# Optimization experiments

Hardware: AMD Instinct MI355X
Metric: run time of the kernel (lower is better)

The kernel has to match this reference:

```python
import jax, jax.numpy as jnp
import numpy as np

B, C_IN, H, W = 8, 64, 128, 128
NUM_POINT = 128
N_INST = 512
INIT_STRIDE, COARSE_STRIDE, DOWN_SAMPLE = 10.0, 4.0, 4.0
D_MODEL, N_HEADS = 256, 8


def conv2d(x, w, b, pad):
    y = jax.lax.conv_general_dilated(x, w, (1, 1), [(pad, pad), (pad, pad)],
                                     dimension_numbers=('NCHW', 'OIHW', 'NCHW'))
    return y + b[None, :, None, None]


def trans_feature(x, w1, b1, w2, b2):
    # Conv3x3 -> ReLU -> Conv1x1 (c_in -> 256 -> 254)
    return conv2d(jax.nn.relu(conv2d(x, w1, b1, 1)), w2, b2, 0)


def grid_sample_points(feat, img_idx, pts):
    # get_gcn_feature: per-instance bilinear sampling of feat[img_idx] at pixel
    # coords pts. torch grid_sample(align_corners=False, padding_mode='zeros');
    # the normalize->unnormalize of pixel coords collapses to a -0.5 shift.
    Bf, C, Hf, Wf = feat.shape
    ix = pts[..., 0] - 0.5
    iy = pts[..., 1] - 0.5
    x0 = jnp.floor(ix)
    y0 = jnp.floor(iy)
    wx = ix - x0
    wy = iy - y0

    def gather(yy, xx, wgt):
        valid = (xx >= 0) & (xx < Wf) & (yy >= 0) & (yy < Hf)
        xc = jnp.clip(xx, 0, Wf - 1).astype(jnp.int32)
        yc = jnp.clip(yy, 0, Hf - 1).astype(jnp.int32)
        v = feat[img_idx[:, None], :, yc, xc]  # [N,P,C]
        return v * (wgt * valid)[..., None]

    return (gather(y0, x0, (1 - wx) * (1 - wy)) + gather(y0, x0 + 1, wx * (1 - wy))
            + gather(y0 + 1, x0, (1 - wx) * wy) + gather(y0 + 1, x0 + 1, wx * wy))


def normalize_poly(poly):
    # Center each contour and scale by its max extent -> positional encoding in [-1,1]
    mean = poly.mean(axis=1, keepdims=True)
    p = poly - mean
    scale = jnp.max(jnp.abs(p), axis=(1, 2), keepdims=True) + 1e-6
    return p / scale


def csa(x, wqkv, bqkv, wo, bo, whead, bhead):
    # ContourSelfAttention: MHSA over contour points + linear head to 2D offsets
    N, P, C = x.shape
    d = C // N_HEADS
    qkv = x @ wqkv + bqkv
    q, k, v = jnp.split(qkv, 3, axis=-1)
    sh = lambda t: t.reshape(N, P, N_HEADS, d).transpose(0, 2, 1, 3)
    q, k, v = sh(q), sh(k), sh(v)
    attn = jax.nn.softmax(jnp.einsum('nhpd,nhqd->nhpq', q, k) / jnp.sqrt(jnp.float32(d)), axis=-1)
    o = jnp.einsum('nhpq,nhqd->nhpd', attn, v).transpose(0, 2, 1, 3).reshape(N, P, C)
    o = o @ wo + bo
    return o @ whead + bhead  # [N,P,2]


def setup_inputs():
    key = jax.random.key(0)
    ks = jax.random.split(key, 32)
    s = 0.05
    inp = {
        'cnn_feature': jax.random.normal(ks[0], (B, C_IN, H, W), jnp.float32),
        'wh_pred': jax.random.normal(ks[1], (B, 2 * NUM_POINT, H, W), jnp.float32),
        'ct_ind': jax.random.randint(ks[2], (N_INST,), 0, H * W),
        'ct_img_idx': jax.random.randint(ks[3], (N_INST,), 0, B),
    }
    p = lambda i, shape: jax.random.normal(ks[i], shape, jnp.float32) * s
    for pre, i0 in (('f1', 4), ('f2', 8)):
        inp[pre + '_w1'] = p(i0, (256, C_IN, 3, 3))
        inp[pre + '_b1'] = p(i0 + 1, (256,))
        inp[pre + '_w2'] = p(i0 + 2, (254, 256, 1, 1))
        inp[pre + '_b2'] = p(i0 + 3, (254,))
    for pre, i0 in (('csa1', 12), ('csa2', 18)):
        inp[pre + '_wqkv'] = p(i0, (D_MODEL, 3 * D_MODEL))
        inp[pre + '_bqkv'] = p(i0 + 1, (3 * D_MODEL,))
        inp[pre + '_wo'] = p(i0 + 2, (D_MODEL, D_MODEL))
        inp[pre + '_bo'] = p(i0 + 3, (D_MODEL,))
        inp[pre + '_whead'] = p(i0 + 4, (D_MODEL, 2))
        inp[pre + '_bhead'] = p(i0 + 5, (2,))
    return inp


def reference(cnn_feature, wh_pred, ct_ind, ct_img_idx,
              f1_w1, f1_b1, f1_w2, f1_b2, f2_w1, f2_b1, f2_w2, f2_b2,
              csa1_wqkv, csa1_bqkv, csa1_wo, csa1_bo, csa1_whead, csa1_bhead,
              csa2_wqkv, csa2_bqkv, csa2_wo, csa2_bo, csa2_whead, csa2_bhead):
    # ---- Decode.train_decode ----
    ct_x = ct_ind % W
    ct_y = ct_ind // W
    # per-instance gather of contour offsets: wh_pred[img, :, y, x] -> [N, 2*P]
    ct_offset = wh_pred[ct_img_idx, :, ct_y, ct_x].reshape(-1, NUM_POINT, 2)
    ct = jnp.stack([ct_x, ct_y], axis=1).astype(jnp.float32)  # [N,2]
    init_polys = ct_offset * INIT_STRIDE + ct[:, None, :]     # [N,128,2]
    # ---- Refine ----
    feat1 = trans_feature(cnn_feature, f1_w1, f1_b1, f1_w2, f1_b2)  # [B,254,H,W]
    feat2 = trans_feature(cnn_feature, f2_w1, f2_b1, f2_w2, f2_b2)
    points = jnp.concatenate([ct[:, None, :], init_polys], axis=1)  # [N,129,2]
    fp1 = grid_sample_points(feat1, ct_img_idx, points)             # [N,129,254]
    x1 = jnp.concatenate([fp1, normalize_poly(points)], axis=-1)    # [N,129,256]
    offsets1 = csa(x1, csa1_wqkv, csa1_bqkv, csa1_wo, csa1_bo, csa1_whead, csa1_bhead)[:, 1:, :]
    coarse_polys = offsets1 * COARSE_STRIDE + jax.lax.stop_gradient(init_polys)
    fp2 = grid_sample_points(feat2, ct_img_idx, coarse_polys)       # [N,128,254]
    x2 = jnp.concatenate([fp2, normalize_poly(coarse_polys)], axis=-1)
    offsets2 = csa(x2, csa2_wqkv, csa2_bqkv, csa2_wo, csa2_bo, csa2_whead, csa2_bhead)
    final_polys = offsets2 + jax.lax.stop_gradient(coarse_polys)
    return (init_polys * DOWN_SAMPLE, coarse_polys * DOWN_SAMPLE, final_polys * DOWN_SAMPLE)
```

## Files before the change

### kernel.cpp

```cpp
#include <hip/hip_runtime.h>
#include <hip/hip_bf16.h>

typedef unsigned short u16;
typedef unsigned int   u32;
typedef float  f32x4 __attribute__((ext_vector_type(4)));
typedef short  s16x8 __attribute__((ext_vector_type(8)));

__device__ __forceinline__ float bf2f(u16 u) {
    return __uint_as_float(((unsigned int)u) << 16);
}
__device__ __forceinline__ u16 f2bf(float f) {
    unsigned int x = __float_as_uint(f);
    unsigned int r = x + 0x7fffu + ((x >> 16) & 1u);
    return (u16)(r >> 16);
}

#define WIMG 128
#define HIMG 128
#define PADW 130
#define BIMG 8
#define CIN  64
#define NPOINT 128
#define NINST 512

#define AS1 __attribute__((address_space(1)))
#define AS3 __attribute__((address_space(3)))
__device__ __forceinline__ void async16(const void* g, void* l) {
    __builtin_amdgcn_global_load_lds((const AS1 void*)g, (AS3 void*)l, 16, 0, 0);
}

__global__ __launch_bounds__(256) void k_cvt_w1(const float* __restrict__ w,
                                                u16* __restrict__ wb) {
    int idx = blockIdx.x * 256 + threadIdx.x;
    int oc = idx / 576, r = idx % 576;
    int kp = r >> 6, ic = r & 63;
    wb[idx] = f2bf(w[oc * 576 + ic * 9 + kp]);
}

__global__ __launch_bounds__(256) void k_cvt_w2(const float* __restrict__ w,
                                                u16* __restrict__ wb) {
    int idx = blockIdx.x * 256 + threadIdx.x;
    int oc = idx >> 8, ic = idx & 255;
    wb[idx] = (oc < 254) ? f2bf(w[oc * 256 + ic]) : (u16)0;
}

__global__ __launch_bounds__(256) void k_cvt_wqkv(const float* __restrict__ w,
                                                  u16* __restrict__ wb) {
    int idx = blockIdx.x * 256 + threadIdx.x;
    int n = idx >> 8, k = idx & 255;
    wb[idx] = f2bf(w[k * 768 + n]);
}

__global__ __launch_bounds__(256) void k_headfuse(const float* __restrict__ wo,
                                                  const float* __restrict__ bo,
                                                  const float* __restrict__ whead,
                                                  const float* __restrict__ bhead,
                                                  float* __restrict__ W2,
                                                  float* __restrict__ b2) {
    int idx = blockIdx.x * 256 + threadIdx.x;
    if (idx < 512) {
        int c = idx >> 1, j = idx & 1;
        float s = 0.f;
        for (int t = 0; t < 256; ++t)
            s = fmaf(wo[c * 256 + t], whead[t * 2 + j], s);
        W2[idx] = s;
    }
    if (idx < 2) {
        float s = bhead[idx];
        for (int t = 0; t < 256; ++t)
            s = fmaf(bo[t], whead[t * 2 + idx], s);
        b2[idx] = s;
    }
}

__global__ __launch_bounds__(256) void k_zero(u16* __restrict__ p) {
    int i = blockIdx.x * 256 + threadIdx.x;
    ((uint4*)p)[i] = make_uint4(0u, 0u, 0u, 0u);
}

__global__ __launch_bounds__(256) void k_nhwc(const float* __restrict__ in,
                                              u16* __restrict__ out) {
    __shared__ u16 sT[128][80];
    int b = blockIdx.x >> 7, y = blockIdx.x & 127;
    int tid = threadIdx.x;
    const float* ib = in + ((size_t)b * CIN * HIMG + y) * WIMG;
    int x4 = tid & 31, icg = tid >> 5;
    #pragma unroll
    for (int pass = 0; pass < 8; ++pass) {
        int ic = pass * 8 + icg;
        float4 v = *(const float4*)&ib[(size_t)ic * (HIMG * WIMG) + x4 * 4];
        sT[x4 * 4 + 0][ic] = f2bf(v.x);
        sT[x4 * 4 + 1][ic] = f2bf(v.y);
        sT[x4 * 4 + 2][ic] = f2bf(v.z);
        sT[x4 * 4 + 3][ic] = f2bf(v.w);
    }
    __syncthreads();
    u16* ob = out + ((size_t)(b * PADW + y + 1) * PADW + 1) * 64;
    int icu = tid & 7, xw = tid >> 3;
    #pragma unroll
    for (int pass = 0; pass < 4; ++pass) {
        int x = pass * 32 + xw;
        uint4 v = *(const uint4*)&sT[x][icu * 8];
        *(uint4*)&ob[(size_t)x * 64 + icu * 8] = v;
    }
}

__global__ __launch_bounds__(256) void k_init(const float* __restrict__ whp,
                                              const int* __restrict__ ct_ind,
                                              const int* __restrict__ ct_img,
                                              float* __restrict__ points1,
                                              float* __restrict__ out0) {
    int i = blockIdx.x;
    int t = threadIdx.x;
    int ind = ct_ind[i];
    int x = ind % WIMG, y = ind / WIMG;
    int b = ct_img[i];
    int p = t >> 1, c = t & 1;
    float off = whp[(((size_t)b * 2 * NPOINT + t) * HIMG + y) * WIMG + x];
    float ctc = (c == 0) ? (float)x : (float)y;
    float ip = off * 10.0f + ctc;
    points1[((size_t)i * 129 + 1 + p) * 2 + c] = ip;
    if (t < 2) points1[(size_t)i * 129 * 2 + t] = (t == 0) ? (float)x : (float)y;
    out0[((size_t)i * NPOINT + p) * 2 + c] = ip * 4.0f;
}

__global__ __launch_bounds__(512) void k_convgemm(const u16* __restrict__ inTp,
                                                  const u16* __restrict__ wb1,
                                                  const float* __restrict__ b1,
                                                  const u16* __restrict__ wb2,
                                                  const float* __restrict__ b2,
                                                  u16* __restrict__ feat) {
    __shared__ u16 smem[50176];
    u16* sB = smem;
    u16* sA = smem + 16384;
    u16* sC = smem + 16384;

    int tid = threadIdx.x;
    int wave = tid >> 6, lane = tid & 63;
    int quad = lane >> 4, l16 = lane & 15;
    int rl = lane >> 2, part = lane & 3;
    int bx = blockIdx.x;
    int y = (bx & 7) * 16 + (bx >> 3);
    int b = blockIdx.z;
    int wm = (wave >> 1) * 32, wn = (wave & 1) * 128;
    const u16* inb = inTp + (size_t)b * PADW * PADW * 64;

    f32x4 acc[2][8];
    #pragma unroll
    for (int mt = 0; mt < 2; ++mt)
        #pragma unroll
        for (int nt = 0; nt < 8; ++nt)
            #pragma unroll
            for (int q = 0; q < 4; ++q) acc[mt][nt][q] = 0.f;

    auto stageA = [&](u16* dst, int t) {
        int kp = t >> 1, ic0 = (t & 1) << 5;
        int ky = kp / 3, kx = kp - ky * 3;
        const u16* arow = inb + ((size_t)(y + ky) * PADW + kx) * 64 + ic0;
        int rr = wave * 16;
        async16(arow + (size_t)(rr + rl) * 64 + part * 8, dst + rr * 32);
    };
    auto stageB1 = [&](u16* dst, int t) {
        int kp = t >> 1, ic0 = (t & 1) << 5;
        const u16* brow = wb1 + (size_t)kp * 64 + ic0;
        #pragma unroll
        for (int j = 0; j < 2; ++j) {
            int rr = wave * 32 + j * 16;
            async16(brow + (size_t)(rr + rl) * 576 + part * 8, dst + rr * 32);
        }
    };
    auto stageB2 = [&](u16* dst, int kk) {
        #pragma unroll
        for (int j = 0; j < 2; ++j) {
            int rr = wave * 32 + j * 16;
            async16(wb2 + (size_t)(rr + rl) * 256 + kk + part * 8, dst + rr * 32);
        }
    };

    stageA(sA, 0);
    stageB1(sB, 0);
    __syncthreads();
    int buf = 0;
    for (int t = 0; t < 18; ++t) {
        if (t < 17) {
            stageA(sA + (buf ^ 1) * 4096, t + 1);
            stageB1(sB + (buf ^ 1) * 8192, t + 1);
        }
        s16x8 aF[2], bF[8];
        #pragma unroll
        for (int mt = 0; mt < 2; ++mt)
            aF[mt] = *(const s16x8*)&sA[buf * 4096 + (wm + mt * 16 + l16) * 32 + quad * 8];
        #pragma unroll
        for (int nt = 0; nt < 8; ++nt)
            bF[nt] = *(const s16x8*)&sB[buf * 8192 + (wn + nt * 16 + l16) * 32 + quad * 8];
        #pragma unroll
        for (int mt = 0; mt < 2; ++mt)
            #pragma unroll
            for (int nt = 0; nt < 8; ++nt)
                acc[mt][nt] = __builtin_amdgcn_mfma_f32_16x16x32_bf16(
                    aF[mt], bF[nt], acc[mt][nt], 0, 0, 0);
        __syncthreads();
        buf ^= 1;
    }

    #pragma unroll
    for (int nt = 0; nt < 8; ++nt) {
        int col = wn + nt * 16 + l16;
        float bv = b1[col];
        #pragma unroll
        for (int mt = 0; mt < 2; ++mt) {
            #pragma unroll
            for (int r = 0; r < 4; ++r) {
                int row = wm + mt * 16 + quad * 4 + r;
                sC[row * 264 + col] = f2bf(fmaxf(acc[mt][nt][r] + bv, 0.f));
            }
        }
    }
    stageB2(sB, 0);
    __syncthreads();

    #pragma unroll
    for (int mt = 0; mt < 2; ++mt)
        #pragma unroll
        for (int nt = 0; nt < 8; ++nt)
            #pragma unroll
            for (int q = 0; q < 4; ++q) acc[mt][nt][q] = 0.f;
    buf = 0;
    for (int ik = 0; ik < 8; ++ik) {
        if (ik < 7) stageB2(sB + (buf ^ 1) * 8192, (ik + 1) * 32);
        s16x8 aF[2], bF[8];
        #pragma unroll
        for (int mt = 0; mt < 2; ++mt)
            aF[mt] = *(const s16x8*)&sC[(wm + mt * 16 + l16) * 264 + ik * 32 + quad * 8];
        #pragma unroll
        for (int nt = 0; nt < 8; ++nt)
            bF[nt] = *(const s16x8*)&sB[buf * 8192 + (wn + nt * 16 + l16) * 32 + quad * 8];
        #pragma unroll
        for (int mt = 0; mt < 2; ++mt)
            #pragma unroll
            for (int nt = 0; nt < 8; ++nt)
                acc[mt][nt] = __builtin_amdgcn_mfma_f32_16x16x32_bf16(
                    aF[mt], bF[nt], acc[mt][nt], 0, 0, 0);
        __syncthreads();
        buf ^= 1;
    }

    #pragma unroll
    for (int nt = 0; nt < 8; ++nt) {
        int col = wn + nt * 16 + l16;
        float bv = (col < 254) ? b2[col] : 0.f;
        #pragma unroll
        for (int mt = 0; mt < 2; ++mt) {
            #pragma unroll
            for (int r = 0; r < 4; ++r) {
                int row = wm + mt * 16 + quad * 4 + r;
                sC[row * 264 + col] = f2bf(acc[mt][nt][r] + bv);
            }
        }
    }
    __syncthreads();
    u16* outb = feat + ((size_t)b * (HIMG * WIMG) + (size_t)y * 128) * 256;
    #pragma unroll
    for (int it = 0; it < 8; ++it) {
        int idx = it * 512 + tid;
        int row = idx >> 5, ch = idx & 31;
        *(uint4*)&outb[(size_t)row * 256 + ch * 8] = *(const uint4*)&sC[row * 264 + ch * 8];
    }
}

__global__ __launch_bounds__(256) void k_gemm_mfma(const u16* __restrict__ A,
                                                   const u16* __restrict__ Bt,
                                                   const float* __restrict__ bias, int nbias,
                                                   u16* __restrict__ C,
                                                   int M, int N, int K, int relu) {
    __shared__ u16 sA[2][128 * 32];
    __shared__ u16 sB[2][128 * 32];
    __shared__ u16 sOut[64 * 132];
    int tid = threadIdx.x;
    int wave = tid >> 6, lane = tid & 63;
    int quad = lane >> 4, l16 = lane & 15;
    int rl = lane >> 2, part = lane & 3;
    int r0 = wave * 32;

    int gx = gridDim.x, gy = gridDim.y;
    int o = blockIdx.y * gx + blockIdx.x;
    int nwg = gx * gy;
    int qn = nwg >> 3, r8 = nwg & 7;
    int xcd = o & 7, oi = o >> 3;
    int vid = (xcd < r8) ? xcd * (qn + 1) + oi : r8 * (qn + 1) + (xcd - r8) * qn + oi;
    int m0 = (vid / gy) * 128, n0 = (vid % gy) * 128;
    int wm = (wave >> 1) * 64, wn = (wave & 1) * 64;

    f32x4 acc[4][4];
    #pragma unroll
    for (int a = 0; a < 4; ++a)
        #pragma unroll
        for (int b = 0; b < 4; ++b)
            #pragma unroll
            for (int q = 0; q < 4; ++q) acc[a][b][q] = 0.f;

    auto stage = [&](int bufi, int kk) {
        #pragma unroll
        for (int j = 0; j < 2; ++j) {
            int rr = r0 + j * 16;
            async16(&A[(size_t)(m0 + rr + rl) * K + kk + part * 8], &sA[bufi][rr * 32]);
            async16(&Bt[(size_t)(n0 + rr + rl) * K + kk + part * 8], &sB[bufi][rr * 32]);
        }
    };

    stage(0, 0);
    __syncthreads();
    int buf = 0;
    int nk = K >> 5;
    for (int ik = 0; ik < nk; ++ik) {
        if (ik + 1 < nk) stage(buf ^ 1, (ik + 1) << 5);
        s16x8 aF[4], bF[4];
        #pragma unroll
        for (int mt = 0; mt < 4; ++mt)
            aF[mt] = *(const s16x8*)&sA[buf][(wm + mt * 16 + l16) * 32 + quad * 8];
        #pragma unroll
        for (int nt = 0; nt < 4; ++nt)
            bF[nt] = *(const s16x8*)&sB[buf][(wn + nt * 16 + l16) * 32 + quad * 8];
        #pragma unroll
        for (int mt = 0; mt < 4; ++mt)
            #pragma unroll
            for (int nt = 0; nt < 4; ++nt)
                acc[mt][nt] = __builtin_amdgcn_mfma_f32_16x16x32_bf16(
                    aF[mt], bF[nt], acc[mt][nt], 0, 0, 0);
        __syncthreads();
        buf ^= 1;
    }

    #pragma unroll
    for (int pass = 0; pass < 2; ++pass) {
        __syncthreads();
        if ((wave >> 1) == pass) {
            #pragma unroll
            for (int nt = 0; nt < 4; ++nt) {
                int col = wn + nt * 16 + l16;
                int gcol = n0 + col;
                float bv = (gcol < nbias) ? bias[gcol] : 0.f;
                #pragma unroll
                for (int mt = 0; mt < 4; ++mt) {
                    #pragma unroll
                    for (int r = 0; r < 4; ++r) {
                        int rowl = mt * 16 + quad * 4 + r;
                        float v = acc[mt][nt][r] + bv;
                        if (relu) v = fmaxf(v, 0.f);
                        sOut[rowl * 132 + col] = f2bf(v);
                    }
                }
            }
        }
        __syncthreads();
        #pragma unroll
        for (int it = 0; it < 8; ++it) {
            int idx = it * 256 + tid;
            int rowl = idx >> 5, ch = idx & 31;
            *(uint2*)&C[(size_t)(m0 + pass * 64 + rowl) * N + n0 + ch * 4] =
                *(const uint2*)&sOut[rowl * 132 + ch * 4];
        }
    }
}

__global__ __launch_bounds__(256) void k_norm(const float* __restrict__ pts,
                                              u16* __restrict__ xout, int P) {
    int i = blockIdx.x, t = threadIdx.x;
    __shared__ float sx[256], sy[256];
    float px = 0.f, py = 0.f;
    if (t < P) {
        px = pts[((size_t)i * P + t) * 2 + 0];
        py = pts[((size_t)i * P + t) * 2 + 1];
    }
    sx[t] = px; sy[t] = py;
    __syncthreads();
    for (int s = 128; s > 0; s >>= 1) {
        if (t < s) { sx[t] += sx[t + s]; sy[t] += sy[t + s]; }
        __syncthreads();
    }
    float mx = sx[0] / (float)P, my = sy[0] / (float)P;
    __syncthreads();
    float ax = 0.f;
    if (t < P) ax = fmaxf(fabsf(px - mx), fabsf(py - my));
    sx[t] = ax;
    __syncthreads();
    for (int s = 128; s > 0; s >>= 1) {
        if (t < s) sx[t] = fmaxf(sx[t], sx[t + s]);
        __syncthreads();
    }
    float scale = sx[0] + 1e-6f;
    if (t < P) {
        size_t base = ((size_t)i * P + t) * 256;
        xout[base + 254] = f2bf((px - mx) / scale);
        xout[base + 255] = f2bf((py - my) / scale);
    }
}

__global__ __launch_bounds__(256) void k_sample(const u16* __restrict__ feat,
                                                const float* __restrict__ pts,
                                                const int* __restrict__ ct_img,
                                                u16* __restrict__ xout, int P) {
    int i = blockIdx.x;
    int p = blockIdx.y * 2 + (threadIdx.x >> 7);
    int c0 = (threadIdx.x & 127) * 2;
    if (p >= P || c0 >= 254) return;
    float px = pts[((size_t)i * P + p) * 2 + 0];
    float py = pts[((size_t)i * P + p) * 2 + 1];
    int b = ct_img[i];
    float ix = px - 0.5f, iy = py - 0.5f;
    float x0f = floorf(ix), y0f = floorf(iy);
    float wx = ix - x0f, wy = iy - y0f;
    int x0 = (int)x0f, y0 = (int)y0f;
    float a0 = 0.f, a1 = 0.f;
    #pragma unroll
    for (int dy = 0; dy < 2; ++dy) {
        #pragma unroll
        for (int dx = 0; dx < 2; ++dx) {
            int xx = x0 + dx, yy = y0 + dy;
            float w = (dx ? wx : 1.f - wx) * (dy ? wy : 1.f - wy);
            if (xx >= 0 && xx < WIMG && yy >= 0 && yy < HIMG) {
                u32 v = *(const u32*)&feat[(((size_t)b * HIMG + yy) * WIMG + xx) * 256 + c0];
                a0 = fmaf(w, bf2f((u16)(v & 0xffffu)), a0);
                a1 = fmaf(w, bf2f((u16)(v >> 16)), a1);
            }
        }
    }
    u32 st = (u32)f2bf(a0) | ((u32)f2bf(a1) << 16);
    *(u32*)&xout[((size_t)i * P + p) * 256 + c0] = st;
}

__global__ __launch_bounds__(256) void k_attn_mfma(const u16* __restrict__ qkv,
                                                   u16* __restrict__ obuf,
                                                   int P) {
    __shared__ u16 smem[144 * 40 * 2 + 32 * 168];
    u16* sQ = smem;
    u16* sK = smem + 144 * 40;
    u16* sVT = smem + 2 * 144 * 40;

    int il = blockIdx.x, h = blockIdx.y;
    int tid = threadIdx.x;
    int wave = tid >> 6, lane = tid & 63;
    int quad = lane >> 4, l16 = lane & 15;

    {
        u32* z = (u32*)smem;
        for (int i = tid; i < (144 * 40 * 2 + 32 * 168) / 2; i += 256) z[i] = 0u;
    }
    __syncthreads();
    for (int idx = tid; idx < 129 * 16 && (idx >> 4) < P; idx += 256) {
        int row = idx >> 4, c2 = idx & 15;
        size_t gb = ((size_t)il * P + row) * 768 + h * 32 + c2 * 2;
        *(u32*)&sQ[row * 40 + c2 * 2] = *(const u32*)&qkv[gb];
        *(u32*)&sK[row * 40 + c2 * 2] = *(const u32*)&qkv[gb + 256];
        u32 v = *(const u32*)&qkv[gb + 512];
        int kin = row & 31;
        int pcol = (row & ~31) + ((kin >> 2) & 3) * 8 + (kin >> 4) * 4 + (kin & 3);
        int d0 = c2 * 2;
        sVT[d0 * 168 + pcol] = (u16)(v & 0xffffu);
        sVT[(d0 + 1) * 168 + pcol] = (u16)(v >> 16);
    }
    __syncthreads();

    const float scale = 0.17677669529663689f;
    for (int qt = wave; qt < 9; qt += 4) {
        s16x8 bq = *(const s16x8*)&sQ[(qt * 16 + l16) * 40 + quad * 8];
        f32x4 s4[9];
        #pragma unroll
        for (int kt = 0; kt < 9; ++kt) {
            s16x8 aK = *(const s16x8*)&sK[(kt * 16 + l16) * 40 + quad * 8];
            f32x4 zz = {0.f, 0.f, 0.f, 0.f};
            s4[kt] = __builtin_amdgcn_mfma_f32_16x16x32_bf16(aK, bq, zz, 0, 0, 0);
        }
        float mx = -1e30f;
        #pragma unroll
        for (int kt = 0; kt < 9; ++kt)
            #pragma unroll
            for (int r = 0; r < 4; ++r) {
                int k = kt * 16 + quad * 4 + r;
                float v = (k < P) ? s4[kt][r] * scale : -1e30f;
                s4[kt][r] = v;
                mx = fmaxf(mx, v);
            }
        mx = fmaxf(mx, __shfl_xor(mx, 16));
        mx = fmaxf(mx, __shfl_xor(mx, 32));
        float l = 0.f;
        #pragma unroll
        for (int kt = 0; kt < 9; ++kt)
            #pragma unroll
            for (int r = 0; r < 4; ++r) {
                float e = __expf(s4[kt][r] - mx);
                s4[kt][r] = e;
                l += e;
            }
        l += __shfl_xor(l, 16);
        l += __shfl_xor(l, 32);
        u16 pb[9][4];
        #pragma unroll
        for (int kt = 0; kt < 9; ++kt)
            #pragma unroll
            for (int r = 0; r < 4; ++r) pb[kt][r] = f2bf(s4[kt][r]);
        f32x4 o[2];
        #pragma unroll
        for (int mt = 0; mt < 2; ++mt)
            #pragma unroll
            for (int q = 0; q < 4; ++q) o[mt][q] = 0.f;
        #pragma unroll
        for (int t = 0; t < 5; ++t) {
            s16x8 bp;
            #pragma unroll
            for (int j = 0; j < 4; ++j) bp[j] = (short)pb[2 * t][j];
            #pragma unroll
            for (int j = 0; j < 4; ++j)
                bp[4 + j] = (2 * t + 1 < 9) ? (short)pb[2 * t + 1][j] : (short)0;
            #pragma unroll
            for (int mt = 0; mt < 2; ++mt) {
                s16x8 aV = *(const s16x8*)&sVT[(mt * 16 + l16) * 168 + t * 32 + quad * 8];
                o[mt] = __builtin_amdgcn_mfma_f32_16x16x32_bf16(aV, bp, o[mt], 0, 0, 0);
            }
        }
        int q = qt * 16 + l16;
        if (q < P) {
            float inv = 1.f / l;
            size_t ob = ((size_t)il * P + q) * 256 + h * 32;
            #pragma unroll
            for (int mt = 0; mt < 2; ++mt) {
                ushort4 st;
                st.x = f2bf(o[mt][0] * inv);
                st.y = f2bf(o[mt][1] * inv);
                st.z = f2bf(o[mt][2] * inv);
                st.w = f2bf(o[mt][3] * inv);
                *(ushort4*)&obuf[ob + mt * 16 + quad * 4] = st;
            }
        }
    }
}

__global__ __launch_bounds__(256) void k_head1(const u16* __restrict__ obuf,
                                               const float* __restrict__ W2,
                                               const float* __restrict__ b2,
                                               const float* __restrict__ pts1,
                                               float* __restrict__ coarse,
                                               float* __restrict__ out1) {
    int wave = threadIdx.x >> 6, lane = threadIdx.x & 63;
    int m = blockIdx.x * 4 + wave;
    const u16* orow = obuf + (size_t)m * 256;
    ushort4 u = *(const ushort4*)(orow + lane * 4);
    float4 w0 = *(const float4*)(W2 + lane * 8);
    float4 w1 = *(const float4*)(W2 + lane * 8 + 4);
    float c0 = bf2f(u.x), c1 = bf2f(u.y), c2 = bf2f(u.z), c3 = bf2f(u.w);
    float s0 = c0 * w0.x + c1 * w0.z + c2 * w1.x + c3 * w1.z;
    float s1 = c0 * w0.y + c1 * w0.w + c2 * w1.y + c3 * w1.w;
    for (int off = 32; off > 0; off >>= 1) {
        s0 += __shfl_down(s0, off);
        s1 += __shfl_down(s1, off);
    }
    if (lane == 0) {
        int i = m / 129, p = m % 129;
        if (p > 0) {
            float o0 = s0 + b2[0], o1 = s1 + b2[1];
            float i0 = pts1[(size_t)m * 2 + 0];
            float i1 = pts1[(size_t)m * 2 + 1];
            float cc0 = o0 * 4.f + i0, cc1 = o1 * 4.f + i1;
            size_t cm = (size_t)i * 128 + (p - 1);
            coarse[cm * 2 + 0] = cc0;
            coarse[cm * 2 + 1] = cc1;
            out1[cm * 2 + 0] = cc0 * 4.f;
            out1[cm * 2 + 1] = cc1 * 4.f;
        }
    }
}

__global__ __launch_bounds__(256) void k_head2(const u16* __restrict__ obuf,
                                               const float* __restrict__ W2,
                                               const float* __restrict__ b2,
                                               const float* __restrict__ coarse,
                                               float* __restrict__ out2) {
    int wave = threadIdx.x >> 6, lane = threadIdx.x & 63;
    int m = blockIdx.x * 4 + wave;
    const u16* orow = obuf + (size_t)m * 256;
    ushort4 u = *(const ushort4*)(orow + lane * 4);
    float4 w0 = *(const float4*)(W2 + lane * 8);
    float4 w1 = *(const float4*)(W2 + lane * 8 + 4);
    float c0 = bf2f(u.x), c1 = bf2f(u.y), c2 = bf2f(u.z), c3 = bf2f(u.w);
    float s0 = c0 * w0.x + c1 * w0.z + c2 * w1.x + c3 * w1.z;
    float s1 = c0 * w0.y + c1 * w0.w + c2 * w1.y + c3 * w1.w;
    for (int off = 32; off > 0; off >>= 1) {
        s0 += __shfl_down(s0, off);
        s1 += __shfl_down(s1, off);
    }
    if (lane == 0) {
        float f0 = s0 + b2[0] + coarse[(size_t)m * 2 + 0];
        float f1 = s1 + b2[1] + coarse[(size_t)m * 2 + 1];
        out2[(size_t)m * 2 + 0] = f0 * 4.f;
        out2[(size_t)m * 2 + 1] = f1 * 4.f;
    }
}

extern "C" void kernel_launch(void* const* d_in, const int* in_sizes, int n_in,
                              void* d_out, int out_size, void* d_ws, size_t ws_size,
                              hipStream_t stream) {
    const float* cnn     = (const float*)d_in[0];
    const float* whp     = (const float*)d_in[1];
    const int*   ct_ind  = (const int*)d_in[2];
    const int*   ct_img  = (const int*)d_in[3];
    const float* f1_w1   = (const float*)d_in[4];
    const float* f1_b1   = (const float*)d_in[5];
    const float* f1_w2   = (const float*)d_in[6];
    const float* f1_b2   = (const float*)d_in[7];
    const float* f2_w1   = (const float*)d_in[8];
    const float* f2_b1   = (const float*)d_in[9];
    const float* f2_w2   = (const float*)d_in[10];
    const float* f2_b2   = (const float*)d_in[11];
    const float* c1_wqkv = (const float*)d_in[12];
    const float* c1_bqkv = (const float*)d_in[13];
    const float* c1_wo   = (const float*)d_in[14];
    const float* c1_bo   = (const float*)d_in[15];
    const float* c1_wh   = (const float*)d_in[16];
    const float* c1_bh   = (const float*)d_in[17];
    const float* c2_wqkv = (const float*)d_in[18];
    const float* c2_bqkv = (const float*)d_in[19];
    const float* c2_wo   = (const float*)d_in[20];
    const float* c2_bo   = (const float*)d_in[21];
    const float* c2_wh   = (const float*)d_in[22];
    const float* c2_bh   = (const float*)d_in[23];

    char* ws = (char*)d_ws;
    float* points1 = (float*)(ws + 0);
    float* coarse  = (float*)(ws + 528384);
    float* W2_1    = (float*)(ws + 1052672);
    float* b2_1    = (float*)(ws + 1054720);
    float* W2_2    = (float*)(ws + 1054976);
    float* b2_2    = (float*)(ws + 1057024);
    u16*   wb1a    = (u16*)(ws + 1057280);
    u16*   wb1b    = (u16*)(ws + 1352192);
    u16*   wb2a    = (u16*)(ws + 1647104);
    u16*   wb2b    = (u16*)(ws + 1778176);
    u16*   wqT1    = (u16*)(ws + 1909248);
    u16*   wqT2    = (u16*)(ws + 2302464);
    u16*   inT     = (u16*)(ws + 2695680);
    u16*   feat    = (u16*)(ws + 20001280);
    u16*   xbuf    = (u16*)(ws + 87110144);
    u16*   qkv_all = (u16*)(ws + 120926720);

    float* out0 = (float*)d_out;
    float* out1 = out0 + 131072;
    float* out2 = out0 + 262144;

    k_cvt_w1<<<576, 256, 0, stream>>>(f1_w1, wb1a);
    k_cvt_w1<<<576, 256, 0, stream>>>(f2_w1, wb1b);
    k_cvt_w2<<<256, 256, 0, stream>>>(f1_w2, wb2a);
    k_cvt_w2<<<256, 256, 0, stream>>>(f2_w2, wb2b);
    k_cvt_wqkv<<<768, 256, 0, stream>>>(c1_wqkv, wqT1);
    k_cvt_wqkv<<<768, 256, 0, stream>>>(c2_wqkv, wqT2);
    k_headfuse<<<2, 256, 0, stream>>>(c1_wo, c1_bo, c1_wh, c1_bh, W2_1, b2_1);
    k_headfuse<<<2, 256, 0, stream>>>(c2_wo, c2_bo, c2_wh, c2_bh, W2_2, b2_2);
    k_init<<<NINST, 256, 0, stream>>>(whp, ct_ind, ct_img, points1, out0);
    k_zero<<<4225, 256, 0, stream>>>(inT);
    k_nhwc<<<1024, 256, 0, stream>>>(cnn, inT);

    k_convgemm<<<dim3(128, 1, 8), 512, 0, stream>>>(inT, wb1a, f1_b1, wb2a, f1_b2, feat);
    k_norm<<<NINST, 256, 0, stream>>>(points1, xbuf, 129);
    k_sample<<<dim3(NINST, 65), 256, 0, stream>>>(feat, points1, ct_img, xbuf, 129);
    k_gemm_mfma<<<dim3(516, 6), 256, 0, stream>>>(xbuf, wqT1, c1_bqkv, 768, qkv_all,
                                                  66048, 768, 256, 0);
    k_attn_mfma<<<dim3(NINST, 8), 256, 0, stream>>>(qkv_all, xbuf, 129);
    k_head1<<<16512, 256, 0, stream>>>(xbuf, W2_1, b2_1, points1, coarse, out1);

    k_convgemm<<<dim3(128, 1, 8), 512, 0, stream>>>(inT, wb1b, f2_b1, wb2b, f2_b2, feat);
    k_norm<<<NINST, 256, 0, stream>>>(coarse, xbuf, 128);
    k_sample<<<dim3(NINST, 64), 256, 0, stream>>>(feat, coarse, ct_img, xbuf, 128);
    k_gemm_mfma<<<dim3(512, 6), 256, 0, stream>>>(xbuf, wqT2, c2_bqkv, 768, qkv_all,
                                                  65536, 768, 256, 0);
    k_attn_mfma<<<dim3(NINST, 8), 256, 0, stream>>>(qkv_all, xbuf, 128);
    k_head2<<<16384, 256, 0, stream>>>(xbuf, W2_2, b2_2, coarse, out2);
}
```

Baseline: 773.4 us.

## Restructure conv GEMM to 256 threads with swizzled LDS and split second GEMM

The fused conv3x3+conv1x1 kernel now runs 4 waves per block instead of 8, each computing a larger 64x128 tile. The second 1x1 GEMM is done in two 64-row halves so the intermediate tile and shared memory shrink, allowing two blocks per CU. An XOR swizzle is added to the LDS layouts in both the conv and QKV GEMMs to reduce bank conflicts. The QKV GEMM also reuses one shared buffer for its staging and output tiles to raise occupancy. Larger per-wave accumulators raise register pressure and could cause spills.

```diff
diff --git a/kernel.cpp b/kernel.cpp
--- a/kernel.cpp
+++ b/kernel.cpp
@@ -28,6 +28,7 @@
 __device__ __forceinline__ void async16(const void* g, void* l) {
     __builtin_amdgcn_global_load_lds((const AS1 void*)g, (AS3 void*)l, 16, 0, 0);
 }
+
 
 __global__ __launch_bounds__(256) void k_cvt_w1(const float* __restrict__ w,
                                                 u16* __restrict__ wb) {
@@ -124,13 +125,13 @@
     out0[((size_t)i * NPOINT + p) * 2 + c] = ip * 4.0f;
 }
 
-__global__ __launch_bounds__(512) void k_convgemm(const u16* __restrict__ inTp,
-                                                  const u16* __restrict__ wb1,
-                                                  const float* __restrict__ b1,
-                                                  const u16* __restrict__ wb2,
-                                                  const float* __restrict__ b2,
-                                                  u16* __restrict__ feat) {
-    __shared__ u16 smem[50176];
+__global__ __launch_bounds__(256, 2) void k_convgemm(const u16* __restrict__ inTp,
+                                                     const u16* __restrict__ wb1,
+                                                     const float* __restrict__ b1,
+                                                     const u16* __restrict__ wb2,
+                                                     const float* __restrict__ b2,
+                                                     u16* __restrict__ feat) {
+    __shared__ u16 smem[33280];
     u16* sB = smem;
     u16* sA = smem + 16384;
     u16* sC = smem + 16384;
@@ -139,41 +140,47 @@
     int wave = tid >> 6, lane = tid & 63;
     int quad = lane >> 4, l16 = lane & 15;
     int rl = lane >> 2, part = lane & 3;
+    int partS = part ^ ((rl ^ (rl >> 2)) & 3);
+    int quadS = quad ^ ((l16 ^ (l16 >> 2)) & 3);
+    int wpx = wave >> 1, woc = wave & 1;
+
     int bx = blockIdx.x;
     int y = (bx & 7) * 16 + (bx >> 3);
     int b = blockIdx.z;
-    int wm = (wave >> 1) * 32, wn = (wave & 1) * 128;
     const u16* inb = inTp + (size_t)b * PADW * PADW * 64;
 
-    f32x4 acc[2][8];
+    f32x4 acc1[4][8];
     #pragma unroll
-    for (int mt = 0; mt < 2; ++mt)
+    for (int mt = 0; mt < 4; ++mt)
         #pragma unroll
         for (int nt = 0; nt < 8; ++nt)
             #pragma unroll
-            for (int q = 0; q < 4; ++q) acc[mt][nt][q] = 0.f;
+            for (int q = 0; q < 4; ++q) acc1[mt][nt][q] = 0.f;
 
     auto stageA = [&](u16* dst, int t) {
         int kp = t >> 1, ic0 = (t & 1) << 5;
         int ky = kp / 3, kx = kp - ky * 3;
-        const u16* arow = inb + ((size_t)(y + ky) * PADW + kx) * 64 + ic0;
-        int rr = wave * 16;
-        async16(arow + (size_t)(rr + rl) * 64 + part * 8, dst + rr * 32);
+        const u16* arow = inb + ((size_t)(y + ky) * PADW + kx) * 64 + ic0 + partS * 8;
+        #pragma unroll
+        for (int j = 0; j < 2; ++j) {
+            int rr = wave * 32 + j * 16;
+            async16(arow + (size_t)(rr + rl) * 64, dst + rr * 32);
+        }
     };
     auto stageB1 = [&](u16* dst, int t) {
         int kp = t >> 1, ic0 = (t & 1) << 5;
-        const u16* brow = wb1 + (size_t)kp * 64 + ic0;
-        #pragma unroll
-        for (int j = 0; j < 2; ++j) {
-            int rr = wave * 32 + j * 16;
-            async16(brow + (size_t)(rr + rl) * 576 + part * 8, dst + rr * 32);
+        const u16* brow = wb1 + (size_t)kp * 64 + ic0 + partS * 8;
+        #pragma unroll
+        for (int j = 0; j < 4; ++j) {
+            int rr = wave * 64 + j * 16;
+            async16(brow + (size_t)(rr + rl) * 576, dst + rr * 32);
         }
     };
     auto stageB2 = [&](u16* dst, int kk) {
         #pragma unroll
-        for (int j = 0; j < 2; ++j) {
-            int rr = wave * 32 + j * 16;
-            async16(wb2 + (size_t)(rr + rl) * 256 + kk + part * 8, dst + rr * 32);
+        for (int j = 0; j < 4; ++j) {
+            int rr = wave * 64 + j * 16;
+            async16(wb2 + (size_t)(rr + rl) * 256 + kk + partS * 8, dst + rr * 32);
         }
     };
 
@@ -186,100 +193,111 @@
             stageA(sA + (buf ^ 1) * 4096, t + 1);
             stageB1(sB + (buf ^ 1) * 8192, t + 1);
         }
-        s16x8 aF[2], bF[8];
-        #pragma unroll
-        for (int mt = 0; mt < 2; ++mt)
-            aF[mt] = *(const s16x8*)&sA[buf * 4096 + (wm + mt * 16 + l16) * 32 + quad * 8];
+        s16x8 aF[4], bF[8];
+        #pragma unroll
+        for (int mt = 0; mt < 4; ++mt)
+            aF[mt] = *(const s16x8*)&sA[buf * 4096 + (wpx * 64 + mt * 16 + l16) * 32 + quadS * 8];
         #pragma unroll
         for (int nt = 0; nt < 8; ++nt)
-            bF[nt] = *(const s16x8*)&sB[buf * 8192 + (wn + nt * 16 + l16) * 32 + quad * 8];
-        #pragma unroll
-        for (int mt = 0; mt < 2; ++mt)
+            bF[nt] = *(const s16x8*)&sB[buf * 8192 + (woc * 128 + nt * 16 + l16) * 32 + quadS * 8];
+        #pragma unroll
+        for (int mt = 0; mt < 4; ++mt)
             #pragma unroll
             for (int nt = 0; nt < 8; ++nt)
-                acc[mt][nt] = __builtin_amdgcn_mfma_f32_16x16x32_bf16(
-                    aF[mt], bF[nt], acc[mt][nt], 0, 0, 0);
+                acc1[mt][nt] = __builtin_amdgcn_mfma_f32_16x16x32_bf16(
+                    aF[mt], bF[nt], acc1[mt][nt], 0, 0, 0);
         __syncthreads();
         buf ^= 1;
     }
 
-    #pragma unroll
-    for (int nt = 0; nt < 8; ++nt) {
-        int col = wn + nt * 16 + l16;
-        float bv = b1[col];
-        #pragma unroll
-        for (int mt = 0; mt < 2; ++mt) {
-            #pragma unroll
-            for (int r = 0; r < 4; ++r) {
-                int row = wm + mt * 16 + quad * 4 + r;
-                sC[row * 264 + col] = f2bf(fmaxf(acc[mt][nt][r] + bv, 0.f));
-            }
-        }
-    }
-    stageB2(sB, 0);
-    __syncthreads();
-
-    #pragma unroll
-    for (int mt = 0; mt < 2; ++mt)
-        #pragma unroll
-        for (int nt = 0; nt < 8; ++nt)
-            #pragma unroll
-            for (int q = 0; q < 4; ++q) acc[mt][nt][q] = 0.f;
-    buf = 0;
-    for (int ik = 0; ik < 8; ++ik) {
-        if (ik < 7) stageB2(sB + (buf ^ 1) * 8192, (ik + 1) * 32);
-        s16x8 aF[2], bF[8];
-        #pragma unroll
-        for (int mt = 0; mt < 2; ++mt)
-            aF[mt] = *(const s16x8*)&sC[(wm + mt * 16 + l16) * 264 + ik * 32 + quad * 8];
-        #pragma unroll
-        for (int nt = 0; nt < 8; ++nt)
-            bF[nt] = *(const s16x8*)&sB[buf * 8192 + (wn + nt * 16 + l16) * 32 + quad * 8];
-        #pragma unroll
-        for (int mt = 0; mt < 2; ++mt)
-            #pragma unroll
-            for (int nt = 0; nt < 8; ++nt)
-                acc[mt][nt] = __builtin_amdgcn_mfma_f32_16x16x32_bf16(
-                    aF[mt], bF[nt], acc[mt][nt], 0, 0, 0);
-        __syncthreads();
-        buf ^= 1;
-    }
-
-    #pragma unroll
-    for (int nt = 0; nt < 8; ++nt) {
-        int col = wn + nt * 16 + l16;
-        float bv = (col < 254) ? b2[col] : 0.f;
-        #pragma unroll
-        for (int mt = 0; mt < 2; ++mt) {
-            #pragma unroll
-            for (int r = 0; r < 4; ++r) {
-                int row = wm + mt * 16 + quad * 4 + r;
-                sC[row * 264 + col] = f2bf(acc[mt][nt][r] + bv);
-            }
-        }
-    }
-    __syncthreads();
-    u16* outb = feat + ((size_t)b * (HIMG * WIMG) + (size_t)y * 128) * 256;
-    #pragma unroll
-    for (int it = 0; it < 8; ++it) {
-        int idx = it * 512 + tid;
-        int row = idx >> 5, ch = idx & 31;
-        *(uint4*)&outb[(size_t)row * 256 + ch * 8] = *(const uint4*)&sC[row * 264 + ch * 8];
-    }
-}
-
-__global__ __launch_bounds__(256) void k_gemm_mfma(const u16* __restrict__ A,
-                                                   const u16* __restrict__ Bt,
-                                                   const float* __restrict__ bias, int nbias,
-                                                   u16* __restrict__ C,
-                                                   int M, int N, int K, int relu) {
-    __shared__ u16 sA[2][128 * 32];
-    __shared__ u16 sB[2][128 * 32];
-    __shared__ u16 sOut[64 * 132];
+    u16* outb0 = feat + ((size_t)b * (HIMG * WIMG) + (size_t)y * 128) * 256;
+    #pragma unroll 1
+    for (int half = 0; half < 2; ++half) {
+        if (wpx == half) {
+            #pragma unroll
+            for (int nt = 0; nt < 8; ++nt) {
+                int col = woc * 128 + nt * 16 + l16;
+                float bv = b1[col];
+                #pragma unroll
+                for (int mt = 0; mt < 4; ++mt) {
+                    #pragma unroll
+                    for (int r = 0; r < 4; ++r) {
+                        int row = mt * 16 + quad * 4 + r;
+                        sC[row * 264 + col] = f2bf(fmaxf(acc1[mt][nt][r] + bv, 0.f));
+                    }
+                }
+            }
+        }
+        stageB2(sB, 0);
+        __syncthreads();
+
+        f32x4 acc2[4][4];
+        #pragma unroll
+        for (int mt = 0; mt < 4; ++mt)
+            #pragma unroll
+            for (int nt = 0; nt < 4; ++nt)
+                #pragma unroll
+                for (int q = 0; q < 4; ++q) acc2[mt][nt][q] = 0.f;
+        int b2f = 0;
+        for (int ik = 0; ik < 8; ++ik) {
+            if (ik < 7) stageB2(sB + (b2f ^ 1) * 8192, (ik + 1) * 32);
+            s16x8 a2[4], bb[4];
+            #pragma unroll
+            for (int mt = 0; mt < 4; ++mt)
+                a2[mt] = *(const s16x8*)&sC[(mt * 16 + l16) * 264 + ik * 32 + quad * 8];
+            #pragma unroll
+            for (int nt = 0; nt < 4; ++nt)
+                bb[nt] = *(const s16x8*)&sB[b2f * 8192 + (wave * 64 + nt * 16 + l16) * 32 + quadS * 8];
+            #pragma unroll
+            for (int mt = 0; mt < 4; ++mt)
+                #pragma unroll
+                for (int nt = 0; nt < 4; ++nt)
+                    acc2[mt][nt] = __builtin_amdgcn_mfma_f32_16x16x32_bf16(
+                        a2[mt], bb[nt], acc2[mt][nt], 0, 0, 0);
+            __syncthreads();
+            b2f ^= 1;
+        }
+
+        #pragma unroll
+        for (int nt = 0; nt < 4; ++nt) {
+            int col = wave * 64 + nt * 16 + l16;
+            float bv = (col < 254) ? b2[col] : 0.f;
+            #pragma unroll
+            for (int mt = 0; mt < 4; ++mt) {
+                #pragma unroll
+                for (int r = 0; r < 4; ++r) {
+                    int row = mt * 16 + quad * 4 + r;
+                    sC[row * 264 + col] = f2bf(acc2[mt][nt][r] + bv);
+                }
+            }
+        }
+        __syncthreads();
+        u16* outb = outb0 + (size_t)half * 64 * 256;
+        #pragma unroll
+        for (int it = 0; it < 8; ++it) {
+            int idx = it * 256 + tid;
+            int row = idx >> 5, ch = idx & 31;
+            *(uint4*)&outb[(size_t)row * 256 + ch * 8] = *(const uint4*)&sC[row * 264 + ch * 8];
+        }
+        __syncthreads();
+    }
+}
+
+__global__ __launch_bounds__(256, 4) void k_gemm_mfma(const u16* __restrict__ A,
+                                                      const u16* __restrict__ Bt,
+                                                      const float* __restrict__ bias, int nbias,
+                                                      u16* __restrict__ C,
+                                                      int M, int N, int K, int relu) {
+    __shared__ u16 smem[16384];
+    u16* sA = smem;
+    u16* sB = smem + 8192;
+    u16* sOut = smem;
     int tid = threadIdx.x;
     int wave = tid >> 6, lane = tid & 63;
     int quad = lane >> 4, l16 = lane & 15;
     int rl = lane >> 2, part = lane & 3;
+    int partS = part ^ ((rl ^ (rl >> 2)) & 3);
+    int quadS = quad ^ ((l16 ^ (l16 >> 2)) & 3);
     int r0 = wave * 32;
 
     int gx = gridDim.x, gy = gridDim.y;
@@ -303,8 +321,8 @@
         #pragma unroll
         for (int j = 0; j < 2; ++j) {
             int rr = r0 + j * 16;
-            async16(&A[(size_t)(m0 + rr + rl) * K + kk + part * 8], &sA[bufi][rr * 32]);
-            async16(&Bt[(size_t)(n0 + rr + rl) * K + kk + part * 8], &sB[bufi][rr * 32]);
+            async16(&A[(size_t)(m0 + rr + rl) * K + kk + partS * 8], &sA[bufi * 4096 + rr * 32]);
+            async16(&Bt[(size_t)(n0 + rr + rl) * K + kk + partS * 8], &sB[bufi * 4096 + rr * 32]);
         }
     };
 
@@ -317,10 +335,10 @@
         s16x8 aF[4], bF[4];
         #pragma unroll
         for (int mt = 0; mt < 4; ++mt)
-            aF[mt] = *(const s16x8*)&sA[buf][(wm + mt * 16 + l16) * 32 + quad * 8];
+            aF[mt] = *(const s16x8*)&sA[buf * 4096 + (wm + mt * 16 + l16) * 32 + quadS * 8];
         #pragma unroll
         for (int nt = 0; nt < 4; ++nt)
-            bF[nt] = *(const s16x8*)&sB[buf][(wn + nt * 16 + l16) * 32 + quad * 8];
+            bF[nt] = *(const s16x8*)&sB[buf * 4096 + (wn + nt * 16 + l16) * 32 + quadS * 8];
         #pragma unroll
         for (int mt = 0; mt < 4; ++mt)
             #pragma unroll
@@ -333,7 +351,6 @@
 
     #pragma unroll
     for (int pass = 0; pass < 2; ++pass) {
-        __syncthreads();
         if ((wave >> 1) == pass) {
             #pragma unroll
             for (int nt = 0; nt < 4; ++nt) {
@@ -360,6 +377,7 @@
             *(uint2*)&C[(size_t)(m0 + pass * 64 + rowl) * N + n0 + ch * 4] =
                 *(const uint2*)&sOut[rowl * 132 + ch * 4];
         }
+        __syncthreads();
     }
 }
 
@@ -658,7 +676,7 @@
     k_zero<<<4225, 256, 0, stream>>>(inT);
     k_nhwc<<<1024, 256, 0, stream>>>(cnn, inT);
 
-    k_convgemm<<<dim3(128, 1, 8), 512, 0, stream>>>(inT, wb1a, f1_b1, wb2a, f1_b2, feat);
+    k_convgemm<<<dim3(128, 1, 8), 256, 0, stream>>>(inT, wb1a, f1_b1, wb2a, f1_b2, feat);
     k_norm<<<NINST, 256, 0, stream>>>(points1, xbuf, 129);
     k_sample<<<dim3(NINST, 65), 256, 0, stream>>>(feat, points1, ct_img, xbuf, 129);
     k_gemm_mfma<<<dim3(516, 6), 256, 0, stream>>>(xbuf, wqT1, c1_bqkv, 768, qkv_all,
@@ -666,7 +684,7 @@
     k_attn_mfma<<<dim3(NINST, 8), 256, 0, stream>>>(qkv_all, xbuf, 129);
     k_head1<<<16512, 256, 0, stream>>>(xbuf, W2_1, b2_1, points1, coarse, out1);
 
-    k_convgemm<<<dim3(128, 1, 8), 512, 0, stream>>>(inT, wb1b, f2_b1, wb2b, f2_b2, feat);
+    k_convgemm<<<dim3(128, 1, 8), 256, 0, stream>>>(inT, wb1b, f2_b1, wb2b, f2_b2, feat);
     k_norm<<<NINST, 256, 0, stream>>>(coarse, xbuf, 128);
     k_sample<<<dim3(NINST, 64), 256, 0, stream>>>(feat, coarse, ct_img, xbuf, 128);
     k_gemm_mfma<<<dim3(512, 6), 256, 0, stream>>>(xbuf, wqT2, c2_bqkv, 768, qkv_all,
```

After: 856.2 us. +10.7%, slower.
